# Kernel optimization log

Hardware: AMD Instinct MI355X
Metric: run time of the kernel (lower is better)

## Reference

```python
import jax, jax.numpy as jnp
import numpy as np
import math

NUM_V = 32; NUM_K = 16; DK = 128; DV = 128; KCONV = 4; H = 2048
KEY_DIM = NUM_K * DK          # 2048
VALUE_DIM = NUM_V * DV        # 4096
CONV_DIM = 2 * KEY_DIM + VALUE_DIM  # 8192
EPS = 1e-6
VPK = NUM_V // NUM_K


def setup_inputs() -> dict:
    key = jax.random.key(0)
    ks = jax.random.split(key, 12)
    s = 0.02  # weight scale for numerical sanity
    return {
        "hidden_in": jax.random.normal(ks[0], (1, 1, H), jnp.float32),
        "conv_state": jax.random.normal(ks[1], (1, CONV_DIM, KCONV), jnp.float32),
        "rec_state": jax.random.normal(ks[2], (1, NUM_V, DK, DV), jnp.float32) * s,
        "W_qkv": jax.random.normal(ks[3], (CONV_DIM, H), jnp.float32) * s,
        "W_z": jax.random.normal(ks[4], (VALUE_DIM, H), jnp.float32) * s,
        "W_b": jax.random.normal(ks[5], (NUM_V, H), jnp.float32) * s,
        "W_a": jax.random.normal(ks[6], (NUM_V, H), jnp.float32) * s,
        "W_out": jax.random.normal(ks[7], (H, VALUE_DIM), jnp.float32) * s,
        "conv_w": jax.random.normal(ks[8], (CONV_DIM, KCONV), jnp.float32) * s,
        "dt_bias": jax.random.normal(ks[9], (NUM_V,), jnp.float32),
        "A_log": jax.random.normal(ks[10], (NUM_V,), jnp.float32),
        "norm_w": jnp.ones((DV,), jnp.float32),
    }


def _l2norm(x, eps=1e-6):
    return x * jax.lax.rsqrt(jnp.sum(x * x, axis=-1, keepdims=True) + eps)


def reference(hidden_in, conv_state, rec_state, W_qkv, W_z, W_b, W_a,
              W_out, conv_w, dt_bias, A_log, norm_w):
    h = hidden_in[0, 0]                       # (H,)
    mixed = W_qkv @ h                         # (CONV_DIM,)
    z = W_z @ h                               # (VALUE_DIM,)
    b = W_b @ h                               # (NUM_V,)
    a = W_a @ h                               # (NUM_V,)

    # causal conv1d update: shift state by one, take dot with kernel
    w = jnp.concatenate([conv_state, mixed[None, :, None]], axis=-1)  # (1, C, K+1)
    new_conv_state = w[:, :, 1:]                                      # (1, C, K)
    conv_out = jax.nn.silu(jnp.sum(new_conv_state * conv_w[None], axis=-1))[0]  # (C,)

    q = conv_out[:KEY_DIM].reshape(NUM_K, DK)
    k = conv_out[KEY_DIM:2 * KEY_DIM].reshape(NUM_K, DK)
    v = conv_out[2 * KEY_DIM:].reshape(NUM_V, DV)
    q = jnp.repeat(q, VPK, axis=0)            # (NUM_V, DK)
    k = jnp.repeat(k, VPK, axis=0)

    q = _l2norm(q) * (1.0 / math.sqrt(DK))
    k = _l2norm(k)

    beta = jax.nn.sigmoid(b)                                  # (NUM_V,)
    g = -jnp.exp(A_log) * jax.nn.softplus(a + dt_bias)        # (NUM_V,)

    # gated delta-rule recurrent update
    rec = rec_state[0] * jnp.exp(g)[:, None, None]            # (NUM_V, DK, DV)
    kv_mem = jnp.einsum('hkd,hk->hd', rec, k)                 # (NUM_V, DV)
    delta = (v - kv_mem) * beta[:, None]
    rec = rec + k[:, :, None] * delta[:, None, :]
    core = jnp.einsum('hkd,hk->hd', rec, q)                   # (NUM_V, DV)

    # gated RMSNorm over Dv per head
    var = jnp.mean(core * core, axis=-1, keepdims=True)
    xn = core * jax.lax.rsqrt(var + EPS) * norm_w
    zf = z.reshape(NUM_V, DV)
    out = (xn * jax.nn.silu(zf)).reshape(VALUE_DIM)

    hidden_out = (W_out @ out).reshape(1, 1, H)
    return (hidden_out, new_conv_state, rec[None])
```

## Files before the change

### kernel.cpp

```cpp
#include <hip/hip_runtime.h>

#define HDIM 2048
#define NUM_V 32
#define NUM_K 16
#define DK 128
#define DV 128
#define KEY_DIM 2048
#define VALUE_DIM 4096
#define CONV_DIM 8192
#define TOTAL_ROWS 12352



typedef __attribute__((ext_vector_type(4))) float f32x4;

__device__ __forceinline__ f32x4 ntload4(const float* p) {
    return __builtin_nontemporal_load(reinterpret_cast<const f32x4*>(p));
}

__global__ __launch_bounds__(256) void k1_gemv(
    const float* __restrict__ h,
    const float* __restrict__ Wqkv,
    const float* __restrict__ Wz,
    const float* __restrict__ Wb,
    const float* __restrict__ Wa,
    const float* __restrict__ conv_state,
    const float* __restrict__ conv_w,
    float* __restrict__ ws,
    float* __restrict__ out_conv)
{
    const int pair = (blockIdx.x * 256 + threadIdx.x) >> 6;
    const int lane = threadIdx.x & 63;
    if (pair >= TOTAL_ROWS / 2) return;
    const int row0 = pair * 2;

    const float* w0;
    if (row0 < 8192)       w0 = Wqkv + (size_t)row0 * HDIM;
    else if (row0 < 12288) w0 = Wz   + (size_t)(row0 - 8192) * HDIM;
    else if (row0 < 12320) w0 = Wb   + (size_t)(row0 - 12288) * HDIM;
    else                   w0 = Wa   + (size_t)(row0 - 12320) * HDIM;
    const float* w1 = w0 + HDIM;

    float acc0 = 0.f, acc1 = 0.f;
#pragma unroll
    for (int i = 0; i < 8; ++i) {
        const int idx = (i * 64 + lane) * 4;
        f32x4 h4 = *reinterpret_cast<const f32x4*>(h + idx);
        f32x4 a4 = ntload4(w0 + idx);
        f32x4 b4 = ntload4(w1 + idx);
        acc0 += a4.x * h4.x + a4.y * h4.y + a4.z * h4.z + a4.w * h4.w;
        acc1 += b4.x * h4.x + b4.y * h4.y + b4.z * h4.z + b4.w * h4.w;
    }
#pragma unroll
    for (int off = 32; off > 0; off >>= 1) {
        acc0 += __shfl_down(acc0, off, 64);
        acc1 += __shfl_down(acc1, off, 64);
    }

    if (lane == 0) {
        if (row0 < 8192) {
            f32x4 cs0 = *reinterpret_cast<const f32x4*>(conv_state + row0 * 4);
            f32x4 cw0 = *reinterpret_cast<const f32x4*>(conv_w + row0 * 4);
            f32x4 cs1 = *reinterpret_cast<const f32x4*>(conv_state + row0 * 4 + 4);
            f32x4 cw1 = *reinterpret_cast<const f32x4*>(conv_w + row0 * 4 + 4);
            float pre0 = cs0.y * cw0.x + cs0.z * cw0.y + cs0.w * cw0.z + acc0 * cw0.w;
            float pre1 = cs1.y * cw1.x + cs1.z * cw1.y + cs1.w * cw1.z + acc1 * cw1.w;
            ws[row0]     = pre0 / (1.f + expf(-pre0));
            ws[row0 + 1] = pre1 / (1.f + expf(-pre1));
            f32x4 n0; n0.x = cs0.y; n0.y = cs0.z; n0.z = cs0.w; n0.w = acc0;
            f32x4 n1; n1.x = cs1.y; n1.y = cs1.z; n1.z = cs1.w; n1.w = acc1;
            *reinterpret_cast<f32x4*>(out_conv + row0 * 4)     = n0;
            *reinterpret_cast<f32x4*>(out_conv + row0 * 4 + 4) = n1;
        } else {
            ws[row0]     = acc0;
            ws[row0 + 1] = acc1;
        }
    }
}

__global__ __launch_bounds__(1024) void k2_rec(
    const float* __restrict__ ws,
    const float* __restrict__ rec_in,
    const float* __restrict__ dt_bias,
    const float* __restrict__ A_log,
    const float* __restrict__ norm_w,
    float* __restrict__ rec_out,
    float* __restrict__ out_vec)
{
    __shared__ float s_k[128];
    __shared__ float s_q[128];
    __shared__ float s_delta[128];
    __shared__ float s_part[8][128];
    __shared__ float s_red[4];

    const int hh  = blockIdx.x;
    const int t   = threadIdx.x;
    const int d   = t & 127;
    const int kkb = t >> 7;
    const int kh  = hh >> 1;

    const float bv    = ws[12288 + hh];
    const float av    = ws[12320 + hh];
    const float beta  = 1.f / (1.f + expf(-bv));
    const float x     = av + dt_bias[hh];
    const float sp    = fmaxf(x, 0.f) + log1pf(expf(-fabsf(x)));
    const float decay = expf(-expf(A_log[hh]) * sp);

    float qr = 0.f, kr = 0.f;
    if (t < 128) {
        qr = ws[kh * 128 + d];
        kr = ws[KEY_DIM + kh * 128 + d];
        float sq = qr * qr, sk = kr * kr;
#pragma unroll
        for (int off = 32; off > 0; off >>= 1) {
            sq += __shfl_down(sq, off, 64);
            sk += __shfl_down(sk, off, 64);
        }
        if ((t & 63) == 0) { s_red[t >> 6] = sq; s_red[2 + (t >> 6)] = sk; }
    }
    __syncthreads();
    if (t < 128) {
        const float ssq = s_red[0] + s_red[1];
        const float ssk = s_red[2] + s_red[3];
        s_q[d] = qr * rsqrtf(ssq + 1e-6f) * 0.08838834764831845f;
        s_k[d] = kr * rsqrtf(ssk + 1e-6f);
    }
    __syncthreads();

    const float* rrow = rec_in  + (size_t)hh * (DK * DV) + kkb * 16 * DV;
    float*       wrow = rec_out + (size_t)hh * (DK * DV) + kkb * 16 * DV;

    float kvp = 0.f;
#pragma unroll
    for (int i = 0; i < 16; ++i)
        kvp += rrow[i * DV + d] * s_k[kkb * 16 + i];
    s_part[kkb][d] = kvp;
    __syncthreads();

    if (t < 128) {
        float kv = 0.f;
#pragma unroll
        for (int j = 0; j < 8; ++j) kv += s_part[j][d];
        kv *= decay;
        const float vv = ws[2 * KEY_DIM + hh * 128 + d];
        s_delta[d] = (vv - kv) * beta;
    }
    __syncthreads();

    const float dlt = s_delta[d];
    float corep = 0.f;
#pragma unroll
    for (int i = 0; i < 16; ++i) {
        const float r = rrow[i * DV + d] * decay + s_k[kkb * 16 + i] * dlt;
        wrow[i * DV + d] = r;
        corep += r * s_q[kkb * 16 + i];
    }
    s_part[kkb][d] = corep;
    __syncthreads();

    float core = 0.f;
    if (t < 128) {
#pragma unroll
        for (int j = 0; j < 8; ++j) core += s_part[j][d];
        float sc = core * core;
#pragma unroll
        for (int off = 32; off > 0; off >>= 1)
            sc += __shfl_down(sc, off, 64);
        if ((t & 63) == 0) s_red[t >> 6] = sc;
    }
    __syncthreads();
    if (t < 128) {
        const float ssc = s_red[0] + s_red[1];
        const float xn  = core * rsqrtf(ssc * (1.f / 128.f) + 1e-6f) * norm_w[d];
        const float zv  = ws[8192 + hh * 128 + d];
        out_vec[hh * 128 + d] = xn * (zv / (1.f + expf(-zv)));
    }
}

__global__ __launch_bounds__(256) void k3_out(
    const float* __restrict__ Wout,
    const float* __restrict__ out_vec,
    float* __restrict__ hidden_out)
{
    const int pair = (blockIdx.x * 256 + threadIdx.x) >> 6;
    const int lane = threadIdx.x & 63;
    if (pair >= HDIM / 2) return;
    const int row0 = pair * 2;

    const float* w0 = Wout + (size_t)row0 * VALUE_DIM;
    const float* w1 = w0 + VALUE_DIM;

    float acc0 = 0.f, acc1 = 0.f;
#pragma unroll 4
    for (int i = 0; i < 16; ++i) {
        const int idx = (i * 64 + lane) * 4;
        f32x4 o4 = *reinterpret_cast<const f32x4*>(out_vec + idx);
        f32x4 a4 = ntload4(w0 + idx);
        f32x4 b4 = ntload4(w1 + idx);
        acc0 += a4.x * o4.x + a4.y * o4.y + a4.z * o4.z + a4.w * o4.w;
        acc1 += b4.x * o4.x + b4.y * o4.y + b4.z * o4.z + b4.w * o4.w;
    }
#pragma unroll
    for (int off = 32; off > 0; off >>= 1) {
        acc0 += __shfl_down(acc0, off, 64);
        acc1 += __shfl_down(acc1, off, 64);
    }
    if (lane == 0) {
        hidden_out[row0]     = acc0;
        hidden_out[row0 + 1] = acc1;
    }
}

extern "C" void kernel_launch(void* const* d_in, const int* in_sizes, int n_in,
                              void* d_out, int out_size, void* d_ws, size_t ws_size,
                              hipStream_t stream) {
    const float* hidden_in  = (const float*)d_in[0];
    const float* conv_state = (const float*)d_in[1];
    const float* rec_state  = (const float*)d_in[2];
    const float* W_qkv      = (const float*)d_in[3];
    const float* W_z        = (const float*)d_in[4];
    const float* W_b        = (const float*)d_in[5];
    const float* W_a        = (const float*)d_in[6];
    const float* W_out      = (const float*)d_in[7];
    const float* conv_w     = (const float*)d_in[8];
    const float* dt_bias    = (const float*)d_in[9];
    const float* A_log      = (const float*)d_in[10];
    const float* norm_w     = (const float*)d_in[11];

    float* out = (float*)d_out;
    float* ws  = (float*)d_ws;

    k1_gemv<<<(TOTAL_ROWS / 2) / 4, 256, 0, stream>>>(hidden_in, W_qkv, W_z, W_b, W_a,
                                                      conv_state, conv_w, ws, out + 2048);
    k2_rec<<<NUM_V, 1024, 0, stream>>>(ws, rec_state, dt_bias, A_log, norm_w,
                                       out + 2048 + CONV_DIM * 4, ws + 12352);
    k3_out<<<(HDIM / 2) / 4, 256, 0, stream>>>(W_out, ws + 12352, out);
}
```

Measured before the change: 34.62 us.

## Use regular loads, cache rec rows in registers, one row per wave in out GEMV

```diff
diff --git a/kernel.cpp b/kernel.cpp
--- a/kernel.cpp
+++ b/kernel.cpp
@@ -13,10 +13,6 @@
 
 
 typedef __attribute__((ext_vector_type(4))) float f32x4;
-
-__device__ __forceinline__ f32x4 ntload4(const float* p) {
-    return __builtin_nontemporal_load(reinterpret_cast<const f32x4*>(p));
-}
 
 __global__ __launch_bounds__(256) void k1_gemv(
     const float* __restrict__ h,
@@ -46,8 +42,8 @@
     for (int i = 0; i < 8; ++i) {
         const int idx = (i * 64 + lane) * 4;
         f32x4 h4 = *reinterpret_cast<const f32x4*>(h + idx);
-        f32x4 a4 = ntload4(w0 + idx);
-        f32x4 b4 = ntload4(w1 + idx);
+        f32x4 a4 = *reinterpret_cast<const f32x4*>(w0 + idx);
+        f32x4 b4 = *reinterpret_cast<const f32x4*>(w1 + idx);
         acc0 += a4.x * h4.x + a4.y * h4.y + a4.z * h4.z + a4.w * h4.w;
         acc1 += b4.x * h4.x + b4.y * h4.y + b4.z * h4.z + b4.w * h4.w;
     }
@@ -130,10 +126,15 @@
     const float* rrow = rec_in  + (size_t)hh * (DK * DV) + kkb * 16 * DV;
     float*       wrow = rec_out + (size_t)hh * (DK * DV) + kkb * 16 * DV;
 
+    float rv[16];
+#pragma unroll
+    for (int i = 0; i < 16; ++i)
+        rv[i] = rrow[i * DV + d];
+
     float kvp = 0.f;
 #pragma unroll
     for (int i = 0; i < 16; ++i)
-        kvp += rrow[i * DV + d] * s_k[kkb * 16 + i];
+        kvp += rv[i] * s_k[kkb * 16 + i];
     s_part[kkb][d] = kvp;
     __syncthreads();
 
@@ -151,7 +152,7 @@
     float corep = 0.f;
 #pragma unroll
     for (int i = 0; i < 16; ++i) {
-        const float r = rrow[i * DV + d] * decay + s_k[kkb * 16 + i] * dlt;
+        const float r = rv[i] * decay + s_k[kkb * 16 + i] * dlt;
         wrow[i * DV + d] = r;
         corep += r * s_q[kkb * 16 + i];
     }
@@ -182,33 +183,23 @@
     const float* __restrict__ out_vec,
     float* __restrict__ hidden_out)
 {
-    const int pair = (blockIdx.x * 256 + threadIdx.x) >> 6;
+    const int row  = (blockIdx.x * 256 + threadIdx.x) >> 6;
     const int lane = threadIdx.x & 63;
-    if (pair >= HDIM / 2) return;
-    const int row0 = pair * 2;
-
-    const float* w0 = Wout + (size_t)row0 * VALUE_DIM;
-    const float* w1 = w0 + VALUE_DIM;
-
-    float acc0 = 0.f, acc1 = 0.f;
-#pragma unroll 4
+    if (row >= HDIM) return;
+
+    const float* wrow = Wout + (size_t)row * VALUE_DIM;
+    float acc = 0.f;
+#pragma unroll
     for (int i = 0; i < 16; ++i) {
         const int idx = (i * 64 + lane) * 4;
+        f32x4 w4 = *reinterpret_cast<const f32x4*>(wrow + idx);
         f32x4 o4 = *reinterpret_cast<const f32x4*>(out_vec + idx);
-        f32x4 a4 = ntload4(w0 + idx);
-        f32x4 b4 = ntload4(w1 + idx);
-        acc0 += a4.x * o4.x + a4.y * o4.y + a4.z * o4.z + a4.w * o4.w;
-        acc1 += b4.x * o4.x + b4.y * o4.y + b4.z * o4.z + b4.w * o4.w;
-    }
-#pragma unroll
-    for (int off = 32; off > 0; off >>= 1) {
-        acc0 += __shfl_down(acc0, off, 64);
-        acc1 += __shfl_down(acc1, off, 64);
-    }
-    if (lane == 0) {
-        hidden_out[row0]     = acc0;
-        hidden_out[row0 + 1] = acc1;
-    }
+        acc += w4.x * o4.x + w4.y * o4.y + w4.z * o4.z + w4.w * o4.w;
+    }
+#pragma unroll
+    for (int off = 32; off > 0; off >>= 1)
+        acc += __shfl_down(acc, off, 64);
+    if (lane == 0) hidden_out[row] = acc;
 }
 
 extern "C" void kernel_launch(void* const* d_in, const int* in_sizes, int n_in,
@@ -234,5 +225,5 @@
                                                       conv_state, conv_w, ws, out + 2048);
     k2_rec<<<NUM_V, 1024, 0, stream>>>(ws, rec_state, dt_bias, A_log, norm_w,
                                        out + 2048 + CONV_DIM * 4, ws + 12352);
-    k3_out<<<(HDIM / 2) / 4, 256, 0, stream>>>(W_out, ws + 12352, out);
-}
+    k3_out<<<HDIM / 4, 256, 0, stream>>>(W_out, ws + 12352, out);
+}
```

Result: no change. 34.47 us (-0.4%).
